# Performance work log

Hardware: AMD Instinct MI355X
Metric: run time of the kernel (lower is better)

The kernel has to match this reference:

```python
import jax, jax.numpy as jnp
import numpy as np

N, E, IN, HID, OUT = 20000, 640000, 128, 64, 32


def setup_inputs() -> dict:
    key = jax.random.key(0)
    ks = jax.random.split(key, 20)
    nrm = lambda k, sh, s: jax.random.normal(k, sh, jnp.float32) * s
    return {
        "x": nrm(ks[0], (N, IN), 1.0),
        "edge_index": jax.random.randint(ks[1], (2, E), 0, N, dtype=jnp.int32),
        "edge_attr": nrm(ks[2], (E, 1), 1.0),
        # GAT layer 1 (in->hid)
        "W1": nrm(ks[3], (IN, HID), 1.0 / np.sqrt(IN)),
        "a1_src": nrm(ks[4], (HID,), 1.0 / np.sqrt(HID)),
        "a1_dst": nrm(ks[5], (HID,), 1.0 / np.sqrt(HID)),
        "b1": jnp.zeros((HID,), jnp.float32),
        # GAT layer 2 (hid->32)
        "W2": nrm(ks[6], (HID, OUT), 1.0 / np.sqrt(HID)),
        "a2_src": nrm(ks[7], (OUT,), 1.0 / np.sqrt(OUT)),
        "a2_dst": nrm(ks[8], (OUT,), 1.0 / np.sqrt(OUT)),
        "b2": jnp.zeros((OUT,), jnp.float32),
        # LSTM(32,32): gates ordered i,f,g,o as in torch
        "W_ih": nrm(ks[9], (4 * OUT, OUT), 1.0 / np.sqrt(OUT)),
        "W_hh": nrm(ks[10], (4 * OUT, OUT), 1.0 / np.sqrt(OUT)),
        "b_ih": jnp.zeros((4 * OUT,), jnp.float32),
        "b_hh": jnp.zeros((4 * OUT,), jnp.float32),
        # fc1: ReLU -> Linear(32,1)
        "fc1_w": nrm(ks[11], (1, OUT), 1.0 / np.sqrt(OUT)),
        "fc1_b": jnp.zeros((1,), jnp.float32),
        # fc2: Linear(32,16) -> ReLU -> Linear(16,1) -> Sigmoid
        "fc2_w1": nrm(ks[12], (16, OUT), 1.0 / np.sqrt(OUT)),
        "fc2_b1": jnp.zeros((16,), jnp.float32),
        "fc2_w2": nrm(ks[13], (1, 16), 1.0 / np.sqrt(16)),
        "fc2_b2": jnp.zeros((1,), jnp.float32),
    }


def gat_layer(x, src, dst, W, a_src, a_dst, b, n):
    # PyG GATConv (1 head, default): h = xW; e_ij = LeakyReLU(a_src.h_j + a_dst.h_i)
    h = x @ W                              # [n, F]
    es = h @ a_src                          # [n] source scores
    ed = h @ a_dst                          # [n] target scores
    e = jax.nn.leaky_relu(es[src] + ed[dst], 0.2)   # [E']
    m = jax.ops.segment_max(e, dst, num_segments=n)
    p = jnp.exp(e - m[dst])
    denom = jax.ops.segment_sum(p, dst, num_segments=n)
    alpha = p / denom[dst]                  # segment softmax over in-edges of dst
    out = jax.ops.segment_sum(alpha[:, None] * h[src], dst, num_segments=n)
    return out + b


def reference(x, edge_index, edge_attr, W1, a1_src, a1_dst, b1, W2, a2_src,
              a2_dst, b2, W_ih, W_hh, b_ih, b_hh, fc1_w, fc1_b, fc2_w1,
              fc2_b1, fc2_w2, fc2_b2):
    n = x.shape[0]
    # GATConv default add_self_loops=True
    loop = jnp.arange(n, dtype=edge_index.dtype)
    src = jnp.concatenate([edge_index[0], loop])
    dst = jnp.concatenate([edge_index[1], loop])
    # edge_attr unused: GATConv has edge_dim=None
    feats = jax.nn.relu(gat_layer(x, src, dst, W1, a1_src, a1_dst, b1, n))
    feats = gat_layer(feats, src, dst, W2, a2_src, a2_dst, b2, n)   # [n, 32]

    # classification head on mean-pooled features
    x_c = jnp.mean(feats, axis=0)
    x_c = jax.nn.sigmoid(jax.nn.relu(x_c @ fc2_w1.T + fc2_b1) @ fc2_w2.T + fc2_b2)  # (1,)

    # LSTM over node sequence (unbatched, seq_len=n); take final cell state c_n
    def cell(carry, x_t):
        h, c = carry
        z = x_t @ W_ih.T + b_ih + h @ W_hh.T + b_hh
        i, f, g, o = jnp.split(z, 4)
        c = jax.nn.sigmoid(f) * c + jax.nn.sigmoid(i) * jnp.tanh(g)
        h = jax.nn.sigmoid(o) * jnp.tanh(c)
        return (h, c), None

    init = (jnp.zeros((OUT,), feats.dtype), jnp.zeros((OUT,), feats.dtype))
    (h_n, c_n), _ = jax.lax.scan(cell, init, feats)
    x_r = jax.nn.relu(c_n) @ fc1_w.T + fc1_b   # (1,)

    return jnp.stack([x_c, x_r], axis=0)       # (2, 1)
```

## Files before the change

kernel.cpp:

```cpp
#include <hip/hip_runtime.h>

#define IN_F 128
#define HID_F 64
#define OUT_F 32
#define ENC_NEG_INF 0x007FFFFFu
#define LOG2E 1.44269504088896340736f

typedef float f32x2 __attribute__((ext_vector_type(2)));

#define PK_LO(acc, w, hs) \
  asm("v_pk_fma_f32 %0, %1, %2, %0 op_sel_hi:[1,0,1]" : "+v"(acc) : "v"(w), "v"(hs))
#define PK_HI(acc, w, hs) \
  asm("v_pk_fma_f32 %0, %1, %2, %0 op_sel:[0,1,0]" : "+v"(acc) : "v"(w), "v"(hs))

#define OFF_OUT1   0
#define OFF_OUT2   1280000
#define OFF_D1     1920000
#define OFF_D2     1940000
#define OFF_SUM    1960000
#define ZERO_FLOATS 1960064
#define OFF_M1     1960064
#define OFF_M2     1980064
#define OFF_H1     2000064
#define OFF_H2     3280064
#define OFF_ES1    3920064
#define OFF_ED1    3940064
#define OFF_ES2    3960064
#define OFF_ED2    3980064
#define OFF_EBUF   4000064
#define OFF_ZX     4660064

__device__ __forceinline__ unsigned enc_f(float f) {
  unsigned b = __float_as_uint(f);
  return (b & 0x80000000u) ? ~b : (b | 0x80000000u);
}
__device__ __forceinline__ float dec_f(unsigned u) {
  unsigned b = (u & 0x80000000u) ? (u & 0x7FFFFFFFu) : ~u;
  return __uint_as_float(b);
}

template <int CTRL>
__device__ __forceinline__ float qperm(float x) {
  return __uint_as_float((unsigned)__builtin_amdgcn_update_dpp(
      0, (int)__float_as_uint(x), CTRL, 0xF, 0xF, true));
}

__global__ void k_initm(unsigned* __restrict__ m1, unsigned* __restrict__ m2, int n) {
  int i = blockIdx.x * blockDim.x + threadIdx.x;
  if (i < n) { m1[i] = ENC_NEG_INF; m2[i] = ENC_NEG_INF; }
}

__global__ void k_gemm1(const float* __restrict__ x, const float* __restrict__ W1,
                        const float* __restrict__ a_src, const float* __restrict__ a_dst,
                        float* __restrict__ h1, float* __restrict__ es, float* __restrict__ ed) {
  int n = blockIdx.x;
  int f = threadIdx.x;
  const float* xr = x + n * IN_F;
  float acc = 0.f;
#pragma unroll 8
  for (int k = 0; k < IN_F; ++k) acc = fmaf(xr[k], W1[k * HID_F + f], acc);
  h1[n * HID_F + f] = acc;
  float s = acc * a_src[f];
  float d = acc * a_dst[f];
#pragma unroll
  for (int off = 32; off; off >>= 1) {
    s += __shfl_down(s, off, 64);
    d += __shfl_down(d, off, 64);
  }
  if (f == 0) { es[n] = s; ed[n] = d; }
}

__global__ void k_emax(const int* __restrict__ ei, const float* __restrict__ es,
                       const float* __restrict__ ed, float* __restrict__ ebuf,
                       unsigned* __restrict__ menc, int E, int EP) {
  int i = blockIdx.x * blockDim.x + threadIdx.x;
  if (i >= EP) return;
  int src, dst;
  if (i < E) { src = ei[i]; dst = ei[E + i]; } else { src = dst = i - E; }
  float e = es[src] + ed[dst];
  e = (e >= 0.f) ? e : 0.2f * e;
  ebuf[i] = e;
  atomicMax(&menc[dst], enc_f(e));
}

__global__ void k_ep(const int* __restrict__ ei, float* __restrict__ ebuf,
                     const unsigned* __restrict__ menc, float* __restrict__ denom,
                     int E, int EP) {
  int i = blockIdx.x * blockDim.x + threadIdx.x;
  if (i >= EP) return;
  int dst = (i < E) ? ei[E + i] : (i - E);
  float p = __expf(ebuf[i] - dec_f(menc[dst]));
  ebuf[i] = p;
  atomicAdd(&denom[dst], p);
}

template <int F>
__global__ void k_aggr(const int* __restrict__ ei, const float* __restrict__ ebuf,
                       const float* __restrict__ denom, const float* __restrict__ h,
                       float* __restrict__ out, int E, int EP) {
  int gt = blockIdx.x * blockDim.x + threadIdx.x;
  int lane = gt % F;
  int e = gt / F;
  if (e >= EP) return;
  int src, dst;
  if (e < E) { src = ei[e]; dst = ei[E + e]; } else { src = dst = e - E; }
  float alpha = ebuf[e] / denom[dst];
  atomicAdd(&out[dst * F + lane], alpha * h[src * F + lane]);
}

__global__ void k_gemm2(const float* __restrict__ out1, const float* __restrict__ b1,
                        const float* __restrict__ W2, const float* __restrict__ a_src,
                        const float* __restrict__ a_dst, float* __restrict__ h2,
                        float* __restrict__ es, float* __restrict__ ed, int N) {
  int lane = threadIdx.x;
  int f = lane & 31;
  int n = blockIdx.x * 2 + (lane >> 5);
  if (n >= N) return;
  const float* r = out1 + n * HID_F;
  float acc = 0.f;
#pragma unroll 8
  for (int k = 0; k < HID_F; ++k) {
    float v = r[k] + b1[k];
    v = v > 0.f ? v : 0.f;
    acc = fmaf(v, W2[k * OUT_F + f], acc);
  }
  h2[n * OUT_F + f] = acc;
  float s = acc * a_src[f];
  float d = acc * a_dst[f];
#pragma unroll
  for (int off = 16; off; off >>= 1) {
    s += __shfl_down(s, off, 32);
    d += __shfl_down(d, off, 32);
  }
  if (f == 0) { es[n] = s; ed[n] = d; }
}

__global__ void k_zx(const float* __restrict__ out2, const float* __restrict__ b2,
                     const float* __restrict__ Wih, const float* __restrict__ bih,
                     const float* __restrict__ bhh, float* __restrict__ Zx) {
  int r = threadIdx.x;
  int t = blockIdx.x;
  const float* xr = out2 + t * OUT_F;
  float acc = bih[r] + bhh[r];
#pragma unroll
  for (int k = 0; k < OUT_F; ++k) acc = fmaf(xr[k] + b2[k], Wih[r * OUT_F + k], acc);
  float scl = (r >= 64 && r < 96) ? 2.f * LOG2E : LOG2E;
  int pos = ((r & 31) << 2) | (((r >> 5) & 1) << 1) | (r >> 6);
  Zx[t * 128 + pos] = acc * scl;
}

__global__ void k_mean(const float* __restrict__ out2, const float* __restrict__ b2,
                       float* __restrict__ sum, int N) {
  int k = threadIdx.x & 31;
  int row = threadIdx.x >> 5;
  float acc = 0.f;
  for (int n = blockIdx.x * 8 + row; n < N; n += gridDim.x * 8)
    acc += out2[n * OUT_F + k] + b2[k];
  __shared__ float s[256];
  s[threadIdx.x] = acc;
  __syncthreads();
  if (threadIdx.x < 32) {
    float tot = 0.f;
#pragma unroll
    for (int j = 0; j < 8; ++j) tot += s[j * 32 + k];
    atomicAdd(&sum[k], tot);
  }
}

__global__ void k_head(const float* __restrict__ sum, const float* __restrict__ w1,
                       const float* __restrict__ bb1, const float* __restrict__ w2,
                       const float* __restrict__ bb2, float* __restrict__ out, float invN) {
  if (threadIdx.x == 0 && blockIdx.x == 0) {
    float xc[32];
#pragma unroll
    for (int k = 0; k < 32; ++k) xc[k] = sum[k] * invN;
    float t2 = bb2[0];
    for (int j = 0; j < 16; ++j) {
      float a = bb1[j];
#pragma unroll
      for (int k = 0; k < 32; ++k) a = fmaf(w1[j * 32 + k], xc[k], a);
      a = a > 0.f ? a : 0.f;
      t2 = fmaf(w2[j], a, t2);
    }
    out[0] = 1.f / (1.f + __expf(-t2));
  }
}

__global__ void __launch_bounds__(64, 1) k_lstm(
    const float* __restrict__ Zx, const float* __restrict__ Whh,
    const float* __restrict__ fc1w, const float* __restrict__ fc1b,
    float* __restrict__ out, int N) {
  const int l = threadIdx.x;
  const int j = l >> 1;
  const int p = l & 1;
  const int rowA = p * 32 + j;
  const int rowB = (2 + p) * 32 + j;
  const float sclA = LOG2E;
  const float sclB = p ? LOG2E : 2.f * LOG2E;

  f32x2 w2[32];
#pragma unroll
  for (int k = 0; k < 32; ++k) {
    f32x2 w;
    w.x = Whh[rowA * 32 + k] * sclA;
    w.y = Whh[rowB * 32 + k] * sclB;
    w2[k] = w;
  }

  __shared__ float hb[2][64];
  hb[1][l] = 0.f;

  const float2* pz = (const float2*)Zx + l;
  f32x2 zr[8];
#pragma unroll
  for (int s = 0; s < 8; ++s) { float2 v = pz[s * 64]; zr[s].x = v.x; zr[s].y = v.y; }

  const float n2L = -2.f * LOG2E;
  float c = 0.f;
  for (int t = 0; t < N; t += 8) {
#pragma unroll
    for (int s = 0; s < 8; ++s) {
      const int u = t + s;
      f32x2 acc0 = zr[s];
      f32x2 acc1; acc1.x = 0.f; acc1.y = 0.f;
      { float2 v = pz[(u + 8) * 64]; zr[s].x = v.x; zr[s].y = v.y; }
      const f32x2* hbr = (const f32x2*)hb[(u + 1) & 1];
      f32x2 hk2[16];
#pragma unroll
      for (int k2 = 0; k2 < 16; ++k2) hk2[k2] = hbr[k2];
#pragma unroll
      for (int q = 0; q < 8; ++q) {
        PK_LO(acc0, w2[2 * q],      hk2[q]);
        PK_LO(acc1, w2[16 + 2 * q], hk2[8 + q]);
        PK_HI(acc0, w2[2 * q + 1],      hk2[q]);
        PK_HI(acc1, w2[16 + 2 * q + 1], hk2[8 + q]);
      }
      float zA = acc0.x + acc1.x;
      float zB = acc0.y + acc1.y;
      float sA = __builtin_amdgcn_rcpf(1.f + exp2f(-zA));
      float sB = __builtin_amdgcn_rcpf(1.f + exp2f(-zB));
      float fgx = qperm<0xB1>(sA);
      float ogx = qperm<0xB1>(sB);
      float gg = fmaf(2.f, sB, -1.f);
      c = fmaf(fgx, c, sA * gg);
      float r3 = __builtin_amdgcn_rcpf(1.f + exp2f(n2L * c));
      float tc = fmaf(2.f, r3, -1.f);
      float h = ogx * tc;
      hb[u & 1][p * 32 + j] = h;
    }
  }

  float v = (p == 0) ? fmaxf(c, 0.f) * fc1w[j] : 0.f;
#pragma unroll
  for (int off = 32; off; off >>= 1) v += __shfl_down(v, off, 64);
  if (l == 0) out[1] = v + fc1b[0];
}

extern "C" void kernel_launch(void* const* d_in, const int* in_sizes, int n_in,
                              void* d_out, int out_size, void* d_ws, size_t ws_size,
                              hipStream_t stream) {
  const float* x    = (const float*)d_in[0];
  const int*   ei   = (const int*)d_in[1];
  const float* W1   = (const float*)d_in[3];
  const float* a1s  = (const float*)d_in[4];
  const float* a1d  = (const float*)d_in[5];
  const float* b1   = (const float*)d_in[6];
  const float* W2   = (const float*)d_in[7];
  const float* a2s  = (const float*)d_in[8];
  const float* a2d  = (const float*)d_in[9];
  const float* b2   = (const float*)d_in[10];
  const float* Wih  = (const float*)d_in[11];
  const float* Whh  = (const float*)d_in[12];
  const float* bih  = (const float*)d_in[13];
  const float* bhh  = (const float*)d_in[14];
  const float* fc1w = (const float*)d_in[15];
  const float* fc1b = (const float*)d_in[16];
  const float* f2w1 = (const float*)d_in[17];
  const float* f2b1 = (const float*)d_in[18];
  const float* f2w2 = (const float*)d_in[19];
  const float* f2b2 = (const float*)d_in[20];

  const int N  = in_sizes[0] / IN_F;
  const int E  = in_sizes[1] / 2;
  const int EP = E + N;

  float* ws = (float*)d_ws;
  float*    out1  = ws + OFF_OUT1;
  float*    out2  = ws + OFF_OUT2;
  float*    d1    = ws + OFF_D1;
  float*    d2    = ws + OFF_D2;
  float*    sum   = ws + OFF_SUM;
  unsigned* m1    = (unsigned*)(ws + OFF_M1);
  unsigned* m2    = (unsigned*)(ws + OFF_M2);
  float*    h1    = ws + OFF_H1;
  float*    h2    = ws + OFF_H2;
  float*    es1   = ws + OFF_ES1;
  float*    ed1   = ws + OFF_ED1;
  float*    es2   = ws + OFF_ES2;
  float*    ed2   = ws + OFF_ED2;
  float*    ebuf  = ws + OFF_EBUF;
  float*    Zx    = ws + OFF_ZX;

  hipMemsetAsync(d_ws, 0, (size_t)ZERO_FLOATS * 4, stream);
  k_initm<<<(N + 255) / 256, 256, 0, stream>>>(m1, m2, N);

  k_gemm1<<<N, 64, 0, stream>>>(x, W1, a1s, a1d, h1, es1, ed1);
  int eb = (EP + 255) / 256;
  k_emax<<<eb, 256, 0, stream>>>(ei, es1, ed1, ebuf, m1, E, EP);
  k_ep<<<eb, 256, 0, stream>>>(ei, ebuf, m1, d1, E, EP);
  k_aggr<64><<<((size_t)EP * 64 + 255) / 256, 256, 0, stream>>>(ei, ebuf, d1, h1, out1, E, EP);

  k_gemm2<<<(N + 1) / 2, 64, 0, stream>>>(out1, b1, W2, a2s, a2d, h2, es2, ed2, N);
  k_emax<<<eb, 256, 0, stream>>>(ei, es2, ed2, ebuf, m2, E, EP);
  k_ep<<<eb, 256, 0, stream>>>(ei, ebuf, m2, d2, E, EP);
  k_aggr<32><<<((size_t)EP * 32 + 255) / 256, 256, 0, stream>>>(ei, ebuf, d2, h2, out2, E, EP);

  k_zx<<<N, 128, 0, stream>>>(out2, b2, Wih, bih, bhh, Zx);
  k_mean<<<64, 256, 0, stream>>>(out2, b2, sum, N);
  k_head<<<1, 64, 0, stream>>>(sum, f2w1, f2b1, f2w2, f2b2, (float*)d_out, 1.f / (float)N);
  k_lstm<<<1, 64, 0, stream>>>(Zx, Whh, fc1w, fc1b, (float*)d_out, N);
}
```

Before: 5.332 ms.

## Broadcast LSTM hidden state via ds_bpermute and split the K dimension across lane pairs

The serial LSTM recurrence no longer passes h through a double-buffered LDS array with a store then reload each step. Each step now gathers h straight from registers with ds_bpermute. Each lane pair splits the 32-wide dot product in half, every lane computes partial sums for all four gates, and the halves are combined with a quad permute. The Zx layout is reordered so each lane loads the gate pair it owns. This trades the LDS write/read round trip for more permute ops and redundant sigmoid evaluations per lane on the latency-critical path.

```diff
diff --git a/kernel.cpp b/kernel.cpp
--- a/kernel.cpp
+++ b/kernel.cpp
@@ -145,7 +145,7 @@
 #pragma unroll
   for (int k = 0; k < OUT_F; ++k) acc = fmaf(xr[k] + b2[k], Wih[r * OUT_F + k], acc);
   float scl = (r >= 64 && r < 96) ? 2.f * LOG2E : LOG2E;
-  int pos = ((r & 31) << 2) | (((r >> 5) & 1) << 1) | (r >> 6);
+  int pos = ((r & 31) << 2) | (r >> 5);
   Zx[t * 128 + pos] = acc * scl;
 }
 
@@ -193,22 +193,23 @@
   const int l = threadIdx.x;
   const int j = l >> 1;
   const int p = l & 1;
-  const int rowA = p * 32 + j;
-  const int rowB = (2 + p) * 32 + j;
-  const float sclA = LOG2E;
-  const float sclB = p ? LOG2E : 2.f * LOG2E;
-
-  f32x2 w2[32];
-#pragma unroll
-  for (int k = 0; k < 32; ++k) {
-    f32x2 w;
-    w.x = Whh[rowA * 32 + k] * sclA;
-    w.y = Whh[rowB * 32 + k] * sclB;
-    w2[k] = w;
-  }
-
-  __shared__ float hb[2][64];
-  hb[1][l] = 0.f;
+  const int rI = 0 * 32 + j, rF = 1 * 32 + j, rG = 2 * 32 + j, rO = 3 * 32 + j;
+
+  f32x2 wP[16], wQ[16];
+#pragma unroll
+  for (int k = 0; k < 16; ++k) {
+    int kk = p * 16 + k;
+    f32x2 a, b;
+    a.x = Whh[rI * 32 + kk] * LOG2E;
+    a.y = Whh[rF * 32 + kk] * LOG2E;
+    b.x = Whh[rG * 32 + kk] * (2.f * LOG2E);
+    b.y = Whh[rO * 32 + kk] * LOG2E;
+    wP[k] = a; wQ[k] = b;
+  }
+
+  int ba[16];
+#pragma unroll
+  for (int k = 0; k < 16; ++k) ba[k] = p * 128 + k * 8;
 
   const float2* pz = (const float2*)Zx + l;
   f32x2 zr[8];
@@ -216,37 +217,43 @@
   for (int s = 0; s < 8; ++s) { float2 v = pz[s * 64]; zr[s].x = v.x; zr[s].y = v.y; }
 
   const float n2L = -2.f * LOG2E;
-  float c = 0.f;
+  float h = 0.f, c = 0.f;
   for (int t = 0; t < N; t += 8) {
 #pragma unroll
     for (int s = 0; s < 8; ++s) {
       const int u = t + s;
-      f32x2 acc0 = zr[s];
-      f32x2 acc1; acc1.x = 0.f; acc1.y = 0.f;
+      f32x2 accP, accQ;
+      f32x2 zx = zr[s];
+      if (p == 0) { accP = zx; accQ.x = 0.f; accQ.y = 0.f; }
+      else        { accQ = zx; accP.x = 0.f; accP.y = 0.f; }
       { float2 v = pz[(u + 8) * 64]; zr[s].x = v.x; zr[s].y = v.y; }
-      const f32x2* hbr = (const f32x2*)hb[(u + 1) & 1];
-      f32x2 hk2[16];
-#pragma unroll
-      for (int k2 = 0; k2 < 16; ++k2) hk2[k2] = hbr[k2];
+      unsigned hbits = __float_as_uint(h);
+      f32x2 hk2[8];
 #pragma unroll
       for (int q = 0; q < 8; ++q) {
-        PK_LO(acc0, w2[2 * q],      hk2[q]);
-        PK_LO(acc1, w2[16 + 2 * q], hk2[8 + q]);
-        PK_HI(acc0, w2[2 * q + 1],      hk2[q]);
-        PK_HI(acc1, w2[16 + 2 * q + 1], hk2[8 + q]);
+        hk2[q].x = __uint_as_float((unsigned)__builtin_amdgcn_ds_bpermute(ba[2 * q],     (int)hbits));
+        hk2[q].y = __uint_as_float((unsigned)__builtin_amdgcn_ds_bpermute(ba[2 * q + 1], (int)hbits));
       }
-      float zA = acc0.x + acc1.x;
-      float zB = acc0.y + acc1.y;
-      float sA = __builtin_amdgcn_rcpf(1.f + exp2f(-zA));
-      float sB = __builtin_amdgcn_rcpf(1.f + exp2f(-zB));
-      float fgx = qperm<0xB1>(sA);
-      float ogx = qperm<0xB1>(sB);
-      float gg = fmaf(2.f, sB, -1.f);
-      c = fmaf(fgx, c, sA * gg);
+#pragma unroll
+      for (int q = 0; q < 8; ++q) {
+        PK_LO(accP, wP[2 * q],     hk2[q]);
+        PK_LO(accQ, wQ[2 * q],     hk2[q]);
+        PK_HI(accP, wP[2 * q + 1], hk2[q]);
+        PK_HI(accQ, wQ[2 * q + 1], hk2[q]);
+      }
+      float zi = accP.x + qperm<0xB1>(accP.x);
+      float zf = accP.y + qperm<0xB1>(accP.y);
+      float zg = accQ.x + qperm<0xB1>(accQ.x);
+      float zo = accQ.y + qperm<0xB1>(accQ.y);
+      float ig = __builtin_amdgcn_rcpf(1.f + exp2f(-zi));
+      float fg = __builtin_amdgcn_rcpf(1.f + exp2f(-zf));
+      float og = __builtin_amdgcn_rcpf(1.f + exp2f(-zo));
+      float sg = __builtin_amdgcn_rcpf(1.f + exp2f(-zg));
+      float gg = fmaf(2.f, sg, -1.f);
+      c = fmaf(fg, c, ig * gg);
       float r3 = __builtin_amdgcn_rcpf(1.f + exp2f(n2L * c));
       float tc = fmaf(2.f, r3, -1.f);
-      float h = ogx * tc;
-      hb[u & 1][p * 32 + j] = h;
+      h = og * tc;
     }
   }
 
```

After: 9.574 ms. 79.6% more time.
